# Optimization experiments

Measured on AMD Instinct MI355X. Metric: run time of the kernel, lower is better.

Reference implementation:

```python
import jax, jax.numpy as jnp
import numpy as np

N = 100000
E = 1600000
F_IN = 256
H1, C1 = 4, 32          # layer 1: heads=4, out_channels=32, concat=True -> 128
H2, C2 = 1, 16          # layer 2: heads=1, out_channels=nclass=16, concat=False
SLOPE = 0.2             # leaky relu negative slope


def setup_inputs() -> dict:
    key = jax.random.key(0)
    ks = jax.random.split(key, 10)
    x = jax.random.normal(ks[0], (N, F_IN), dtype=jnp.float32)
    row = jax.random.randint(ks[1], (E,), 0, N, dtype=jnp.int32)      # source j
    off = jax.random.randint(ks[2], (E,), 1, N, dtype=jnp.int32)
    col = ((row + off) % N).astype(jnp.int32)                          # target i, no self loops
    edge_index = jnp.stack([row, col])

    def glorot(k, shape, fan_in, fan_out):
        lim = np.sqrt(6.0 / (fan_in + fan_out))
        return jax.random.uniform(k, shape, jnp.float32, -lim, lim)

    W1 = glorot(ks[3], (F_IN, H1 * C1), F_IN, H1 * C1)
    att1 = glorot(ks[4], (1, H1, 2 * C1), H1, 2 * C1)
    b1 = jnp.zeros((H1 * C1,), jnp.float32)
    W2 = glorot(ks[5], (H1 * C1, H2 * C2), H1 * C1, H2 * C2)
    att2 = glorot(ks[6], (1, H2, 2 * C2), H2, 2 * C2)
    b2 = jnp.zeros((C2,), jnp.float32)
    return {"x": x, "edge_index": edge_index, "W1": W1, "att1": att1,
            "b1": b1, "W2": W2, "att2": att2, "b2": b2}


def gcn_norm(edge_index, num_nodes):
    # add_remaining_self_loops + symmetric normalization (GeoLayer.norm)
    loop = jnp.arange(num_nodes, dtype=edge_index.dtype)
    row = jnp.concatenate([edge_index[0], loop])
    col = jnp.concatenate([edge_index[1], loop])
    w = jnp.ones(row.shape[0], jnp.float32)
    deg = jax.ops.segment_sum(w, row, num_segments=num_nodes)
    dinv = jnp.where(deg > 0, jax.lax.rsqrt(deg), 0.0)
    return row, col, dinv[row] * w * dinv[col]


def segment_softmax(alpha, seg, num_segments):
    amax = jax.ops.segment_max(alpha, seg, num_segments=num_segments)
    ex = jnp.exp(alpha - amax[seg])
    denom = jax.ops.segment_sum(ex, seg, num_segments=num_segments)
    return ex / (denom[seg] + 1e-16)


def geo_layer(x, row, col, ew, W, att, b, heads, out_ch, concat):
    n = x.shape[0]
    xt = (x @ W).reshape(n, heads, out_ch)
    x_i = xt[col]                         # [E+N, H, C] target features
    x_j = xt[row]                         # [E+N, H, C] source features
    wl, wr = att[:, :, :out_ch], att[:, :, out_ch:]
    # (cat([x_i,x_j],-1) * att).sum(-1) == (x_i*wl).sum + (x_j*wr).sum
    alpha = (x_i * wl).sum(-1) + (x_j * wr).sum(-1)     # [E+N, H]
    alpha = jnp.where(alpha >= 0, alpha, SLOPE * alpha)  # leaky_relu
    alpha = segment_softmax(alpha, col, n)
    msg = ew[:, None, None] * x_j * alpha[:, :, None]    # [E+N, H, C]
    out = jax.ops.segment_sum(msg, col, num_segments=n)  # scatter-add to targets
    out = out.reshape(n, heads * out_ch) if concat else out.mean(axis=1)
    return out + b


def reference(x, edge_index, W1, att1, b1, W2, att2, b2):
    # norm is identical for both layers (edge_weight=None each time)
    row, col, ew = gcn_norm(edge_index, x.shape[0])
    h = geo_layer(x, row, col, ew, W1, att1, b1, H1, C1, True)
    h = jax.nn.relu(h)
    out = geo_layer(h, row, col, ew, W2, att2, b2, H2, C2, False)
    return out
```

## Files before the change

### kernel.cpp

```cpp
#include <hip/hip_runtime.h>
#include <math.h>

#define TPB 256
#define SEGN 512
#define SCAP 14336
#define CHB 8192
#define CAPC 12288

__device__ __forceinline__ float lrelu(float a){ return a >= 0.f ? a : 0.2f*a; }

typedef __attribute__((ext_vector_type(8))) short bf16x8;
typedef __attribute__((ext_vector_type(4))) float f32x4;

__device__ __forceinline__ unsigned short bfr(float f){
  unsigned u = __float_as_uint(f);
  return (unsigned short)((u + 0x7fffu + ((u >> 16) & 1u)) >> 16);
}

__device__ __forceinline__ void gl_lds16(const void* g, void* l){
  __builtin_amdgcn_global_load_lds(
      (const __attribute__((address_space(1))) void*)g,
      (__attribute__((address_space(3))) void*)l, 16, 0, 0);
}


__global__ __launch_bounds__(256) void k_bucket2(const int* __restrict__ rows, const int* __restrict__ cols,
    int* __restrict__ bcurC, int* __restrict__ bcurR,
    unsigned* __restrict__ ebufC, unsigned short* __restrict__ ebufR, int E, int NSEG2){
  __shared__ int lhist[256];
  __shared__ int lbase[256];
  int tid = threadIdx.x;
  int e0 = blockIdx.x * CHB;
  #pragma unroll 1
  for(int r=0; r<4; r++){
    lhist[tid] = 0;
    __syncthreads();
    int eb = e0 + r*2048;
    unsigned pk[8]; int sg[8], rk[8];
    #pragma unroll
    for(int i=0;i<8;i++){
      int e = eb + i*256 + tid;
      sg[i] = -1;
      if(e < E){
        int cc = cols[e], rr = rows[e];
        sg[i] = cc >> 9;
        pk[i] = ((unsigned)(cc & (SEGN-1)) << 17) | (unsigned)rr;
        rk[i] = atomicAdd(&lhist[sg[i]], 1);
      }
    }
    __syncthreads();
    if(tid < NSEG2){
      int c = lhist[tid];
      lbase[tid] = c ? atomicAdd(&bcurC[tid], c) : 0;
    }
    __syncthreads();
    #pragma unroll
    for(int i=0;i<8;i++)
      if(sg[i] >= 0){
        int p = lbase[sg[i]] + rk[i];
        if(p < CAPC) ebufC[sg[i]*CAPC + p] = pk[i];
      }
    __syncthreads();
  }
  #pragma unroll 1
  for(int r=0; r<4; r++){
    lhist[tid] = 0;
    __syncthreads();
    int eb = e0 + r*2048;
    int sg[8], rk[8]; unsigned short pv[8];
    #pragma unroll
    for(int i=0;i<8;i++){
      int e = eb + i*256 + tid;
      sg[i] = -1;
      if(e < E){
        int rr = rows[e];
        sg[i] = rr >> 9;
        pv[i] = (unsigned short)(rr & (SEGN-1));
        rk[i] = atomicAdd(&lhist[sg[i]], 1);
      }
    }
    __syncthreads();
    if(tid < NSEG2){
      int c = lhist[tid];
      lbase[tid] = c ? atomicAdd(&bcurR[tid], c) : 0;
    }
    __syncthreads();
    #pragma unroll
    for(int i=0;i<8;i++)
      if(sg[i] >= 0){
        int p = lbase[sg[i]] + rk[i];
        if(p < CAPC) ebufR[sg[i]*CAPC + p] = pv[i];
      }
    __syncthreads();
  }
}

__global__ __launch_bounds__(256) void k_cntseg(const int* __restrict__ bcurC, const int* __restrict__ bcurR,
    const unsigned* __restrict__ ebufC, const unsigned short* __restrict__ ebufR,
    int* __restrict__ cnt, float* __restrict__ dinv, int* __restrict__ bsum, int N){
  __shared__ int hc[SEGN];
  __shared__ int hr[SEGN];
  __shared__ int red[256];
  int s = blockIdx.x, tid = threadIdx.x;
  int lo = s*SEGN;
  int nn = min(SEGN, N - lo);
  for(int i=tid; i<SEGN; i+=256){ hc[i] = 0; hr[i] = 0; }
  __syncthreads();
  int cb = s*CAPC;
  int cc = min(bcurC[s], CAPC);
  int rc = min(bcurR[s], CAPC);
  for(int j=tid; j<cc; j+=256) atomicAdd(&hc[ebufC[cb + j] >> 17], 1);
  for(int j=tid; j<rc; j+=256) atomicAdd(&hr[ebufR[cb + j]], 1);
  __syncthreads();
  int tsum = 0;
  for(int i=tid; i<nn; i+=256){
    int c = hc[i] + 1;
    cnt[lo+i]  = c;
    tsum += c;
    dinv[lo+i] = 1.f / sqrtf((float)(hr[i] + 1));
  }
  red[tid] = tsum; __syncthreads();
  for(int off=128; off>0; off>>=1){
    if(tid < off) red[tid] += red[tid+off];
    __syncthreads();
  }
  if(tid == 0) bsum[s] = red[0];
}

__global__ void k_scan_bsum(int* bsum, int NB){
  __shared__ int s[256];
  int t = threadIdx.x;
  int v = (t < NB) ? bsum[t] : 0;
  s[t] = v; __syncthreads();
  for(int off=1; off<256; off<<=1){
    int add = (t >= off) ? s[t-off] : 0;
    __syncthreads();
    s[t] += add;
    __syncthreads();
  }
  if(t < NB) bsum[t] = s[t] - v;
}

__global__ void k_scan_write(const int* __restrict__ cnt, const int* __restrict__ bsum,
                             int* __restrict__ offs, int N){
  __shared__ int sdata[256];
  int t = threadIdx.x;
  int base = blockIdx.x*512 + t*2;
  int v0 = (base   < N) ? cnt[base]   : 0;
  int v1 = (base+1 < N) ? cnt[base+1] : 0;
  int s = v0 + v1;
  sdata[t] = s; __syncthreads();
  int mine = s;
  for(int off=1; off<256; off<<=1){
    int add = (t >= off) ? sdata[t-off] : 0;
    __syncthreads();
    sdata[t] += add;
    __syncthreads();
  }
  int run = sdata[t] - mine + bsum[blockIdx.x];
  if(base < N){
    offs[base] = run; run += v0;
    if(base == N-1) offs[N] = run;
  }
  if(base+1 < N){
    offs[base+1] = run; run += v1;
    if(base+1 == N-1) offs[N] = run;
  }
}

__global__ __launch_bounds__(256) void k_sortfill(const int* __restrict__ offs,
    const int* __restrict__ bcurC, const unsigned* __restrict__ ebuf,
    int* __restrict__ csr, int N){
  __shared__ int lcur[SEGN];
  __shared__ int lbuf[SCAP];
  int s = blockIdx.x, tid = threadIdx.x;
  int lo = s*SEGN;
  int nn = min(SEGN, N - lo);
  int base = offs[lo];
  int total = offs[lo+nn] - base;
  int eb = s*CAPC;
  int ec = min(bcurC[s], CAPC);
  if(total <= SCAP){
    for(int li=tid; li<nn; li+=256){
      int o = offs[lo+li] - base;
      lbuf[o]  = lo + li;
      lcur[li] = o + 1;
    }
    __syncthreads();
    for(int j=tid; j<ec; j+=256){
      unsigned pk = ebuf[eb + j];
      int li  = pk >> 17;
      int row = pk & 0x1FFFF;
      int p = atomicAdd(&lcur[li], 1);
      lbuf[p] = row;
    }
    __syncthreads();
    for(int j=tid; j<total; j+=256) csr[base + j] = lbuf[j];
  } else {
    for(int li=tid; li<nn; li+=256){
      int o = offs[lo+li];
      csr[o] = lo + li;
      lcur[li] = o + 1;
    }
    __syncthreads();
    for(int j=tid; j<ec; j+=256){
      unsigned pk = ebuf[eb + j];
      int li  = pk >> 17;
      int row = pk & 0x1FFFF;
      int p = atomicAdd(&lcur[li], 1);
      csr[p] = row;
    }
  }
}


__global__ void k_prepW(const float* __restrict__ W, short* __restrict__ Whi,
                        short* __restrict__ Wlo){
  int idx = blockIdx.x*256 + threadIdx.x;
  int n = idx >> 8, k = idx & 255;
  float f = W[k*128 + n];
  unsigned short h = bfr(f);
  float hf = __uint_as_float(((unsigned)h) << 16);
  Whi[n*256 + k] = (short)h;
  Wlo[n*256 + k] = (short)bfr(f - hf);
}


#define BUFB 24576
__global__ __launch_bounds__(256) void k_gemm1(
    const float* __restrict__ x,
    const short* __restrict__ Whi, const short* __restrict__ Wlo,
    const float* __restrict__ att1,
    unsigned* __restrict__ xtb, float* __restrict__ sl, float* __restrict__ sr, int N){
  __shared__ __align__(16) char smem[2*BUFB];
  float* fx = (float*)smem;
  float* att_sh = (float*)(smem + 17408);

  int tid = threadIdx.x;
  int n0 = blockIdx.x * 64;
  int w = tid >> 6, l = tid & 63;
  int wm = w & 1, wn = w >> 1;
  int lm = l & 15, lq = l >> 4;

  f32x4 acc[2][4];
  #pragma unroll
  for(int a=0;a<2;a++)
    #pragma unroll
    for(int b=0;b<4;b++) acc[a][b] = (f32x4){0.f,0.f,0.f,0.f};

  int ua0 = (w<<6) | l, ua1 = 256 + ua0;
  int ar0 = ua0 >> 3, as0 = (ua0 & 7) ^ (ar0 & 7);
  int ar1 = ua1 >> 3, as1 = (ua1 & 7) ^ (ar1 & 7);
  const float* gA0 = x + (size_t)min(n0 + ar0, N-1)*256 + as0*4;
  const float* gA1 = x + (size_t)min(n0 + ar1, N-1)*256 + as1*4;
  int ub0 = (w<<6) | l,  ub1 = 256 + ub0;
  int br0 = ub0 >> 2, bs0 = (ub0 & 3) ^ ((br0 >> 1) & 3);
  int br1 = ub1 >> 2, bs1 = (ub1 & 3) ^ ((br1 >> 1) & 3);
  const short* gBh0 = Whi + br0*256 + bs0*8;
  const short* gBh1 = Whi + br1*256 + bs1*8;
  const short* gBl0 = Wlo + br0*256 + bs0*8;
  const short* gBl1 = Wlo + br1*256 + bs1*8;
  int woff = w << 10;

  int offAf[2][2], offB[4];
  #pragma unroll
  for(int mt=0;mt<2;mt++){
    int rr = wm*32 + mt*16 + lm;
    offAf[mt][0] = rr*32 + (((2*lq+0) ^ (rr&7)) << 2);
    offAf[mt][1] = rr*32 + (((2*lq+1) ^ (rr&7)) << 2);
  }
  #pragma unroll
  for(int nt=0;nt<4;nt++){
    int rr = wn*64 + nt*16 + lm;
    offB[nt] = rr*32 + ((lq ^ ((rr>>1)&3)) << 3);
  }

  {
    char* base = smem;
    gl_lds16(gA0,  base          + woff);
    gl_lds16(gA1,  base + 4096   + woff);
    gl_lds16(gBh0, base + 8192   + woff);
    gl_lds16(gBh1, base + 12288  + woff);
    gl_lds16(gBl0, base + 16384  + woff);
    gl_lds16(gBl1, base + 20480  + woff);
  }
  __syncthreads();

  int cur = 0;
  #pragma unroll 1
  for(int c=0;c<8;c++){
    if(c < 7){
      int kf = (c+1) << 5;
      char* base = smem + (cur^1)*BUFB;
      gl_lds16(gA0  + kf, base          + woff);
      gl_lds16(gA1  + kf, base + 4096   + woff);
      gl_lds16(gBh0 + kf, base + 8192   + woff);
      gl_lds16(gBh1 + kf, base + 12288  + woff);
      gl_lds16(gBl0 + kf, base + 16384  + woff);
      gl_lds16(gBl1 + kf, base + 20480  + woff);
    }
    float* Axf = (float*)(smem + cur*BUFB);
    short* Bh  = (short*)(smem + cur*BUFB + 8192);
    short* Bl  = (short*)(smem + cur*BUFB + 16384);
    bf16x8 ah[2], al2[2];
    #pragma unroll
    for(int mt=0;mt<2;mt++){
      float4 f0 = *((const float4*)&Axf[offAf[mt][0]]);
      float4 f1 = *((const float4*)&Axf[offAf[mt][1]]);
      float fa[8] = {f0.x,f0.y,f0.z,f0.w,f1.x,f1.y,f1.z,f1.w};
      #pragma unroll
      for(int j=0;j<8;j++){
        unsigned short hb = bfr(fa[j]);
        float hf = __uint_as_float(((unsigned)hb) << 16);
        ah[mt][j]  = (short)hb;
        al2[mt][j] = (short)bfr(fa[j] - hf);
      }
    }
    #pragma unroll
    for(int nt=0;nt<4;nt++){
      bf16x8 bh = *((bf16x8*)&Bh[offB[nt]]);
      bf16x8 bl = *((bf16x8*)&Bl[offB[nt]]);
      #pragma unroll
      for(int mt=0;mt<2;mt++){
        acc[mt][nt] = __builtin_amdgcn_mfma_f32_16x16x32_bf16(ah[mt],  bh, acc[mt][nt], 0,0,0);
        acc[mt][nt] = __builtin_amdgcn_mfma_f32_16x16x32_bf16(ah[mt],  bl, acc[mt][nt], 0,0,0);
        acc[mt][nt] = __builtin_amdgcn_mfma_f32_16x16x32_bf16(al2[mt], bh, acc[mt][nt], 0,0,0);
      }
    }
    __syncthreads();
    cur ^= 1;
  }

  #pragma unroll
  for(int mt=0;mt<2;mt++){
    #pragma unroll
    for(int v=0;v<4;v++){
      int row = n0 + wm*32 + mt*16 + lq*4 + v;
      if(row < N){
        unsigned p0 = (unsigned)bfr(acc[mt][0][v]) | ((unsigned)bfr(acc[mt][2][v])<<16);
        unsigned p1 = (unsigned)bfr(acc[mt][1][v]) | ((unsigned)bfr(acc[mt][3][v])<<16);
        int jb = wn*32 + lm;
        xtb[(size_t)row*64 + jb]      = p0;
        xtb[(size_t)row*64 + jb + 16] = p1;
      }
    }
  }

  att_sh[tid] = att1[tid];
  #pragma unroll 1
  for(int p=0;p<2;p++){
    __syncthreads();
    if(wn == p){
      #pragma unroll
      for(int mt=0;mt<2;mt++)
        #pragma unroll
        for(int nt=0;nt<4;nt++)
          #pragma unroll
          for(int v=0;v<4;v++)
            fx[(wm*32 + mt*16 + lq*4 + v)*68 + nt*16 + lm] = acc[mt][nt][v];
    }
    __syncthreads();
    if(tid < 128){
      int rloc = tid >> 1, hh = tid & 1;
      int head = p*2 + hh;
      float a = 0.f, b = 0.f;
      #pragma unroll
      for(int c4=0;c4<8;c4++){
        float4 xv  = *((const float4*)&fx[rloc*68 + hh*32 + c4*4]);
        float4 alv = *((const float4*)&att_sh[head*64 + c4*4]);
        float4 arv = *((const float4*)&att_sh[head*64 + 32 + c4*4]);
        a += xv.x*alv.x + xv.y*alv.y + xv.z*alv.z + xv.w*alv.w;
        b += xv.x*arv.x + xv.y*arv.y + xv.z*arv.z + xv.w*arv.w;
      }
      int row = n0 + rloc;
      if(row < N){
        sl[(size_t)row*4 + head] = a;
        sr[(size_t)row*4 + head] = b;
      }
    }
  }
}


__global__ __launch_bounds__(64) void k_agg1(const int* __restrict__ offs, const int* __restrict__ srcs,
    const float* __restrict__ sl, const float* __restrict__ sr, const float* __restrict__ dinv,
    const unsigned* __restrict__ xtb, const float* __restrict__ b1, float* __restrict__ h, int N){
  __shared__ int   s_sh[64];
  __shared__ float w_sh[64*4];
  int n = blockIdx.x;
  if(n >= N) return;
  int lane = threadIdx.x;
  int beg = offs[n], end = offs[n+1];
  int deg = end - beg;
  float4 sln = *((const float4*)(sl + (size_t)n*4));
  int h0 = lane >> 5;
  float den0=0.f,den1=0.f,den2=0.f,den3=0.f;
  float acc0=0.f, acc1=0.f;

  if(deg <= 64){
    int j = beg + lane;
    int s = 0; float wd = 0.f;
    float a0=-1e30f, a1=-1e30f, a2=-1e30f, a3=-1e30f;
    if(j < end){
      s = srcs[j];
      float4 a = *((const float4*)(sr + (size_t)s*4));
      a0 = lrelu(sln.x + a.x);
      a1 = lrelu(sln.y + a.y);
      a2 = lrelu(sln.z + a.z);
      a3 = lrelu(sln.w + a.w);
      wd = dinv[s];
    }
    float m0=a0,m1=a1,m2=a2,m3=a3;
    #pragma unroll
    for(int o=32;o>0;o>>=1){
      m0 = fmaxf(m0, __shfl_xor(m0,o));
      m1 = fmaxf(m1, __shfl_xor(m1,o));
      m2 = fmaxf(m2, __shfl_xor(m2,o));
      m3 = fmaxf(m3, __shfl_xor(m3,o));
    }
    den0 = __expf(a0 - m0);
    den1 = __expf(a1 - m1);
    den2 = __expf(a2 - m2);
    den3 = __expf(a3 - m3);
    s_sh[lane] = s;
    w_sh[lane*4+0] = wd*den0;
    w_sh[lane*4+1] = wd*den1;
    w_sh[lane*4+2] = wd*den2;
    w_sh[lane*4+3] = wd*den3;
    __syncthreads();
    int k = 0;
    for(; k+8<=deg; k+=8){
      int sk[8];
      #pragma unroll
      for(int u=0;u<8;u++) sk[u] = __builtin_amdgcn_readfirstlane(s_sh[k+u]);
      unsigned pv[8];
      #pragma unroll
      for(int u=0;u<8;u++) pv[u] = xtb[(size_t)sk[u]*64 + lane];
      #pragma unroll
      for(int u=0;u<8;u++){
        float2 wv = *((const float2*)&w_sh[(k+u)*4 + h0*2]);
        acc0 += wv.x * __uint_as_float(pv[u] << 16);
        acc1 += wv.y * __uint_as_float(pv[u] & 0xffff0000u);
      }
    }
    for(; k<deg; k++){
      int sk = __builtin_amdgcn_readfirstlane(s_sh[k]);
      unsigned pvv = xtb[(size_t)sk*64 + lane];
      float2 wv = *((const float2*)&w_sh[k*4 + h0*2]);
      acc0 += wv.x * __uint_as_float(pvv << 16);
      acc1 += wv.y * __uint_as_float(pvv & 0xffff0000u);
    }
  } else {
    float m0=-1e30f,m1=-1e30f,m2=-1e30f,m3=-1e30f;
    for(int j=beg+lane; j<end; j+=64){
      int s = srcs[j];
      float4 a = *((const float4*)(sr + (size_t)s*4));
      m0 = fmaxf(m0, lrelu(sln.x + a.x));
      m1 = fmaxf(m1, lrelu(sln.y + a.y));
      m2 = fmaxf(m2, lrelu(sln.z + a.z));
      m3 = fmaxf(m3, lrelu(sln.w + a.w));
    }
    #pragma unroll
    for(int o=32;o>0;o>>=1){
      m0 = fmaxf(m0, __shfl_xor(m0,o));
      m1 = fmaxf(m1, __shfl_xor(m1,o));
      m2 = fmaxf(m2, __shfl_xor(m2,o));
      m3 = fmaxf(m3, __shfl_xor(m3,o));
    }
    for(int c0=beg; c0<end; c0+=64){
      int cnt = min(64, end-c0);
      int j = c0 + lane;
      float e0=0.f,e1=0.f,e2=0.f,e3=0.f, wd=0.f; int s=0;
      if(j<end){
        s = srcs[j];
        float4 a = *((const float4*)(sr + (size_t)s*4));
        e0 = __expf(lrelu(sln.x + a.x) - m0);
        e1 = __expf(lrelu(sln.y + a.y) - m1);
        e2 = __expf(lrelu(sln.z + a.z) - m2);
        e3 = __expf(lrelu(sln.w + a.w) - m3);
        wd = dinv[s];
      }
      den0+=e0; den1+=e1; den2+=e2; den3+=e3;
      s_sh[lane] = s;
      w_sh[lane*4+0] = wd*e0;
      w_sh[lane*4+1] = wd*e1;
      w_sh[lane*4+2] = wd*e2;
      w_sh[lane*4+3] = wd*e3;
      __syncthreads();
      int k = 0;
      for(; k+8<=cnt; k+=8){
        int sk[8];
        #pragma unroll
        for(int u=0;u<8;u++) sk[u] = __builtin_amdgcn_readfirstlane(s_sh[k+u]);
        unsigned pv[8];
        #pragma unroll
        for(int u=0;u<8;u++) pv[u] = xtb[(size_t)sk[u]*64 + lane];
        #pragma unroll
        for(int u=0;u<8;u++){
          float2 wv = *((const float2*)&w_sh[(k+u)*4 + h0*2]);
          acc0 += wv.x * __uint_as_float(pv[u] << 16);
          acc1 += wv.y * __uint_as_float(pv[u] & 0xffff0000u);
        }
      }
      for(; k<cnt; k++){
        int sk = __builtin_amdgcn_readfirstlane(s_sh[k]);
        unsigned pvv = xtb[(size_t)sk*64 + lane];
        float2 wv = *((const float2*)&w_sh[k*4 + h0*2]);
        acc0 += wv.x * __uint_as_float(pvv << 16);
        acc1 += wv.y * __uint_as_float(pvv & 0xffff0000u);
      }
      __syncthreads();
    }
  }
  #pragma unroll
  for(int o=32;o>0;o>>=1){
    den0 += __shfl_xor(den0,o);
    den1 += __shfl_xor(den1,o);
    den2 += __shfl_xor(den2,o);
    den3 += __shfl_xor(den3,o);
  }
  float din = dinv[n];
  int ch0 = (lane < 32) ? lane : lane + 32;
  int ch1 = ch0 + 32;
  float d0 = (lane < 32) ? den0 : den2;
  float d1 = (lane < 32) ? den1 : den3;
  float o0 = din*acc0/(d0 + 1e-16f) + b1[ch0];
  float o1 = din*acc1/(d1 + 1e-16f) + b1[ch1];
  h[(size_t)n*128 + ch0] = o0 > 0.f ? o0 : 0.f;
  h[(size_t)n*128 + ch1] = o1 > 0.f ? o1 : 0.f;
}


__global__ __launch_bounds__(256) void k_gemm2(const float* __restrict__ hmat, const float* __restrict__ W2,
    const float* __restrict__ att2, unsigned* __restrict__ xt2b,
    float* __restrict__ sl2, float* __restrict__ sr2, int N){
  __shared__ float hs[16*132];
  __shared__ float ws[16*132];
  __shared__ float xs[16*16];
  int t = threadIdx.x;
  int n0 = blockIdx.x * 16;
  #pragma unroll
  for(int i=0;i<8;i++){
    int idx = t + 256*i;
    int k = idx >> 4, c = idx & 15;
    ws[c*132 + k] = W2[idx];
  }
  #pragma unroll
  for(int i=0;i<2;i++){
    int idx = t + 256*i;
    int r = idx >> 5, k4 = idx & 31;
    int n = n0 + r;
    float4 v = make_float4(0.f,0.f,0.f,0.f);
    if(n < N) v = ((const float4*)hmat)[(size_t)n*32 + k4];
    *((float4*)&hs[r*132 + k4*4]) = v;
  }
  __syncthreads();
  int r = t >> 4, c = t & 15;
  float acc = 0.f;
  for(int k=0;k<128;k+=4){
    float4 hv = *((const float4*)&hs[r*132+k]);
    float4 wv = *((const float4*)&ws[c*132+k]);
    acc += hv.x*wv.x + hv.y*wv.y + hv.z*wv.z + hv.w*wv.w;
  }
  xs[r*16 + c] = acc;
  __syncthreads();
  int n = n0 + r;
  if(c < 8 && n < N){
    unsigned pk = (unsigned)bfr(xs[r*16+c]) | ((unsigned)bfr(xs[r*16+c+8])<<16);
    xt2b[(size_t)n*8 + c] = pk;
  }
  if(t < 16){
    int nn = n0 + t;
    if(nn < N){
      float a = 0.f, b = 0.f;
      #pragma unroll
      for(int cc=0;cc<16;cc++){ float v = xs[t*16+cc]; a += v*att2[cc]; b += v*att2[16+cc]; }
      sl2[nn] = a; sr2[nn] = b;
    }
  }
}


__global__ __launch_bounds__(64) void k_agg2(const int* __restrict__ offs, const int* __restrict__ srcs,
    const float* __restrict__ sl2, const float* __restrict__ sr2, const float* __restrict__ dinv,
    const unsigned* __restrict__ xt2b, const float* __restrict__ b2, float* __restrict__ out, int N){
  __shared__ int   s_sh[64];
  __shared__ float w_sh[64];
  int n = blockIdx.x;
  if(n >= N) return;
  int lane = threadIdx.x;
  int beg = offs[n], end = offs[n+1];
  int deg = end - beg;
  float sln = sl2[n];
  float den = 0.f, acc0 = 0.f, acc1 = 0.f;
  int grp = lane >> 3, ch = lane & 7;

  if(deg <= 64){
    int j = beg + lane;
    int s = 0; float wd = 0.f; float a = -1e30f;
    if(j < end){
      s = srcs[j];
      a = lrelu(sln + sr2[s]);
      wd = dinv[s];
    }
    float m = a;
    #pragma unroll
    for(int o=32;o>0;o>>=1) m = fmaxf(m, __shfl_xor(m,o));
    float e = __expf(a - m);
    den = e;
    s_sh[lane] = s;
    w_sh[lane] = wd*e;
    __syncthreads();
    for(int k=0;k<deg;k+=8){
      int kk = k + grp;
      if(kk < deg){
        int sk = s_sh[kk];
        float wk = w_sh[kk];
        unsigned pv = xt2b[(size_t)sk*8 + ch];
        acc0 += wk * __uint_as_float(pv << 16);
        acc1 += wk * __uint_as_float(pv & 0xffff0000u);
      }
    }
  } else {
    float m = -1e30f;
    for(int j=beg+lane; j<end; j+=64)
      m = fmaxf(m, lrelu(sln + sr2[srcs[j]]));
    #pragma unroll
    for(int o=32;o>0;o>>=1) m = fmaxf(m, __shfl_xor(m,o));
    for(int c0=beg; c0<end; c0+=64){
      int cnt = min(64, end-c0);
      int j = c0 + lane;
      float e=0.f, wd=0.f; int s=0;
      if(j<end){
        s = srcs[j];
        e = __expf(lrelu(sln + sr2[s]) - m);
        wd = dinv[s];
      }
      den += e;
      s_sh[lane] = s;
      w_sh[lane] = wd*e;
      __syncthreads();
      for(int k=0;k<cnt;k+=8){
        int kk = k + grp;
        if(kk < cnt){
          int sk = s_sh[kk];
          float wk = w_sh[kk];
          unsigned pv = xt2b[(size_t)sk*8 + ch];
          acc0 += wk * __uint_as_float(pv << 16);
          acc1 += wk * __uint_as_float(pv & 0xffff0000u);
        }
      }
      __syncthreads();
    }
  }
  #pragma unroll
  for(int o=32;o>0;o>>=1) den += __shfl_xor(den,o);
  acc0 += __shfl_xor(acc0,8);  acc0 += __shfl_xor(acc0,16);  acc0 += __shfl_xor(acc0,32);
  acc1 += __shfl_xor(acc1,8);  acc1 += __shfl_xor(acc1,16);  acc1 += __shfl_xor(acc1,32);
  if(lane < 8){
    float din = dinv[n];
    out[(size_t)n*16 + lane]     = din*acc0/(den + 1e-16f) + b2[lane];
    out[(size_t)n*16 + lane + 8] = din*acc1/(den + 1e-16f) + b2[lane+8];
  }
}


extern "C" void kernel_launch(void* const* d_in, const int* in_sizes, int n_in,
                              void* d_out, int out_size, void* d_ws, size_t ws_size,
                              hipStream_t stream){
  const float* x    = (const float*)d_in[0];
  const int*   ei   = (const int*)d_in[1];
  const float* W1   = (const float*)d_in[2];
  const float* att1 = (const float*)d_in[3];
  const float* b1   = (const float*)d_in[4];
  const float* W2   = (const float*)d_in[5];
  const float* att2 = (const float*)d_in[6];
  const float* b2   = (const float*)d_in[7];
  int N = in_sizes[0] / 256;
  int E = in_sizes[1] / 2;
  const int* rows = ei;
  const int* cols = ei + E;
  float* out = (float*)d_out;

  int ET    = E + N;
  int NSEG2 = (N + SEGN - 1) / SEGN;

  char* p = (char*)d_ws;
  auto alloc = [&](size_t bytes)->void*{ void* q = p; p += (bytes + 255) & ~(size_t)255; return q; };
  int*      cnt     = (int*)alloc((size_t)N*4);
  int*      offs    = (int*)alloc((size_t)(N+1)*4);
  int*      bsum    = (int*)alloc(256*4);
  int*      bcur    = (int*)alloc(512*4);
  int*      csr     = (int*)alloc((size_t)ET*4);
  float*    dinv    = (float*)alloc((size_t)N*4);
  unsigned* xtb     = (unsigned*)alloc((size_t)N*64*4);
  float*    sl1     = (float*)alloc((size_t)N*16);
  float*    sr1     = (float*)alloc((size_t)N*16);
  float*    hbuf    = (float*)alloc((size_t)N*128*4);
  unsigned* xt2b    = (unsigned*)alloc((size_t)N*8*4);
  float*    sl2     = (float*)alloc((size_t)N*4);
  float*    sr2     = (float*)alloc((size_t)N*4);
  short*    Whi     = (short*)alloc((size_t)128*256*2);
  short*    Wlo     = (short*)alloc((size_t)128*256*2);

  int* bcurC = bcur;
  int* bcurR = bcur + 256;

  unsigned*       ebufC = (unsigned*)xtb;
  unsigned short* ebufR = (unsigned short*)(ebufC + (size_t)NSEG2*CAPC);

  int gB = (E + CHB - 1) / CHB;

  hipMemsetAsync(bcur, 0, 512*4, stream);
  k_bucket2<<<gB, 256, 0, stream>>>(rows, cols, bcurC, bcurR, ebufC, ebufR, E, NSEG2);
  k_cntseg<<<NSEG2, 256, 0, stream>>>(bcurC, bcurR, ebufC, ebufR, cnt, dinv, bsum, N);
  k_scan_bsum<<<1, 256, 0, stream>>>(bsum, NSEG2);
  k_scan_write<<<NSEG2, 256, 0, stream>>>(cnt, bsum, offs, N);
  k_sortfill<<<NSEG2, 256, 0, stream>>>(offs, bcurC, ebufC, csr, N);

  k_prepW<<<128, 256, 0, stream>>>(W1, Whi, Wlo);
  k_gemm1<<<(N + 63)/64, 256, 0, stream>>>(x, Whi, Wlo, att1, xtb, sl1, sr1, N);
  k_agg1<<<N, 64, 0, stream>>>(offs, csr, sl1, sr1, dinv, xtb, b1, hbuf, N);

  k_gemm2<<<(N + 15)/16, 256, 0, stream>>>(hbuf, W2, att2, xt2b, sl2, sr2, N);
  k_agg2<<<N, 64, 0, stream>>>(offs, csr, sl2, sr2, dinv, xt2b, b2, out, N);
}
```

Measured before the change: 414.7 us.

## Fuse layer-2 GEMM into aggregation, merge bucketing passes and scan into sortfill

Three fusions. The layer-2 projection (h @ W2, the attention dot products and the bf16 packing) is computed per node inside k_agg1, so the 128-float hidden matrix is never written to or read back from global memory. The two bucketing passes over the edge list become a single pass that reads rows and cols once. The per-segment offset scan moves into the sortfill kernel, which removes a launch and a reread of offs. The cost is that each 64-thread agg1 block now reads all of W2 from global or cache, does an extra shuffle reduction and two more barriers, and uses more registers, which may reduce occupancy.

Measured after the change: 406.4 us. 1.02x faster.

```diff
diff --git a/kernel.cpp b/kernel.cpp
--- a/kernel.cpp
+++ b/kernel.cpp
@@ -24,72 +24,45 @@
 }
 
 
-__global__ __launch_bounds__(256) void k_bucket2(const int* __restrict__ rows, const int* __restrict__ cols,
+__global__ __launch_bounds__(256) void k_bucketM(const int* __restrict__ rows, const int* __restrict__ cols,
     int* __restrict__ bcurC, int* __restrict__ bcurR,
     unsigned* __restrict__ ebufC, unsigned short* __restrict__ ebufR, int E, int NSEG2){
-  __shared__ int lhist[256];
-  __shared__ int lbase[256];
+  __shared__ int lhC[256], lbC[256], lhR[256], lbR[256];
   int tid = threadIdx.x;
   int e0 = blockIdx.x * CHB;
   #pragma unroll 1
   for(int r=0; r<4; r++){
-    lhist[tid] = 0;
+    lhC[tid] = 0; lhR[tid] = 0;
     __syncthreads();
     int eb = e0 + r*2048;
-    unsigned pk[8]; int sg[8], rk[8];
+    unsigned pk[8]; int sgC[8], rkC[8], sgR[8], rkR[8]; int pvR[8];
     #pragma unroll
     for(int i=0;i<8;i++){
       int e = eb + i*256 + tid;
-      sg[i] = -1;
+      sgC[i] = -1;
       if(e < E){
         int cc = cols[e], rr = rows[e];
-        sg[i] = cc >> 9;
-        pk[i] = ((unsigned)(cc & (SEGN-1)) << 17) | (unsigned)rr;
-        rk[i] = atomicAdd(&lhist[sg[i]], 1);
+        sgC[i] = cc >> 9;
+        pk[i]  = ((unsigned)(cc & (SEGN-1)) << 17) | (unsigned)rr;
+        rkC[i] = atomicAdd(&lhC[sgC[i]], 1);
+        sgR[i] = rr >> 9;
+        pvR[i] = rr & (SEGN-1);
+        rkR[i] = atomicAdd(&lhR[sgR[i]], 1);
       }
     }
     __syncthreads();
     if(tid < NSEG2){
-      int c = lhist[tid];
-      lbase[tid] = c ? atomicAdd(&bcurC[tid], c) : 0;
+      int c = lhC[tid];  lbC[tid] = c  ? atomicAdd(&bcurC[tid], c)  : 0;
+      int c2 = lhR[tid]; lbR[tid] = c2 ? atomicAdd(&bcurR[tid], c2) : 0;
     }
     __syncthreads();
     #pragma unroll
     for(int i=0;i<8;i++)
-      if(sg[i] >= 0){
-        int p = lbase[sg[i]] + rk[i];
-        if(p < CAPC) ebufC[sg[i]*CAPC + p] = pk[i];
-      }
-    __syncthreads();
-  }
-  #pragma unroll 1
-  for(int r=0; r<4; r++){
-    lhist[tid] = 0;
-    __syncthreads();
-    int eb = e0 + r*2048;
-    int sg[8], rk[8]; unsigned short pv[8];
-    #pragma unroll
-    for(int i=0;i<8;i++){
-      int e = eb + i*256 + tid;
-      sg[i] = -1;
-      if(e < E){
-        int rr = rows[e];
-        sg[i] = rr >> 9;
-        pv[i] = (unsigned short)(rr & (SEGN-1));
-        rk[i] = atomicAdd(&lhist[sg[i]], 1);
-      }
-    }
-    __syncthreads();
-    if(tid < NSEG2){
-      int c = lhist[tid];
-      lbase[tid] = c ? atomicAdd(&bcurR[tid], c) : 0;
-    }
-    __syncthreads();
-    #pragma unroll
-    for(int i=0;i<8;i++)
-      if(sg[i] >= 0){
-        int p = lbase[sg[i]] + rk[i];
-        if(p < CAPC) ebufR[sg[i]*CAPC + p] = pv[i];
+      if(sgC[i] >= 0){
+        int p = lbC[sgC[i]] + rkC[i];
+        if(p < CAPC) ebufC[sgC[i]*CAPC + p] = pk[i];
+        int p2 = lbR[sgR[i]] + rkR[i];
+        if(p2 < CAPC) ebufR[sgR[i]*CAPC + p2] = (unsigned short)pvR[i];
       }
     __syncthreads();
   }
@@ -141,50 +114,46 @@
   if(t < NB) bsum[t] = s[t] - v;
 }
 
-__global__ void k_scan_write(const int* __restrict__ cnt, const int* __restrict__ bsum,
-                             int* __restrict__ offs, int N){
-  __shared__ int sdata[256];
-  int t = threadIdx.x;
-  int base = blockIdx.x*512 + t*2;
-  int v0 = (base   < N) ? cnt[base]   : 0;
-  int v1 = (base+1 < N) ? cnt[base+1] : 0;
-  int s = v0 + v1;
-  sdata[t] = s; __syncthreads();
-  int mine = s;
-  for(int off=1; off<256; off<<=1){
-    int add = (t >= off) ? sdata[t-off] : 0;
-    __syncthreads();
-    sdata[t] += add;
-    __syncthreads();
-  }
-  int run = sdata[t] - mine + bsum[blockIdx.x];
-  if(base < N){
-    offs[base] = run; run += v0;
-    if(base == N-1) offs[N] = run;
-  }
-  if(base+1 < N){
-    offs[base+1] = run; run += v1;
-    if(base+1 == N-1) offs[N] = run;
-  }
-}
-
-__global__ __launch_bounds__(256) void k_sortfill(const int* __restrict__ offs,
-    const int* __restrict__ bcurC, const unsigned* __restrict__ ebuf,
+__global__ __launch_bounds__(256) void k_sortfill2(const int* __restrict__ cnt,
+    const int* __restrict__ bsum, const int* __restrict__ bcurC,
+    const unsigned* __restrict__ ebuf, int* __restrict__ offs,
     int* __restrict__ csr, int N){
   __shared__ int lcur[SEGN];
   __shared__ int lbuf[SCAP];
+  __shared__ int sdata[256];
   int s = blockIdx.x, tid = threadIdx.x;
   int lo = s*SEGN;
   int nn = min(SEGN, N - lo);
-  int base = offs[lo];
-  int total = offs[lo+nn] - base;
+  int base = bsum[s];
+  int i0 = tid*2, i1 = i0+1;
+  int v0 = (i0 < nn) ? cnt[lo+i0] : 0;
+  int v1 = (i1 < nn) ? cnt[lo+i1] : 0;
+  int ssum = v0 + v1;
+  sdata[tid] = ssum; __syncthreads();
+  int mine = ssum;
+  for(int off=1; off<256; off<<=1){
+    int add = (tid >= off) ? sdata[tid-off] : 0;
+    __syncthreads();
+    sdata[tid] += add;
+    __syncthreads();
+  }
+  int total = sdata[255];
+  int run0 = sdata[tid] - mine;
+  int run1 = run0 + v0;
   int eb = s*CAPC;
   int ec = min(bcurC[s], CAPC);
   if(total <= SCAP){
-    for(int li=tid; li<nn; li+=256){
-      int o = offs[lo+li] - base;
-      lbuf[o]  = lo + li;
-      lcur[li] = o + 1;
+    if(i0 < nn){
+      offs[lo+i0] = base + run0;
+      lbuf[run0]  = lo + i0;
+      lcur[i0]    = run0 + 1;
+      if(lo+i0 == N-1) offs[N] = base + run0 + v0;
+    }
+    if(i1 < nn){
+      offs[lo+i1] = base + run1;
+      lbuf[run1]  = lo + i1;
+      lcur[i1]    = run1 + 1;
+      if(lo+i1 == N-1) offs[N] = base + run1 + v1;
     }
     __syncthreads();
     for(int j=tid; j<ec; j+=256){
@@ -197,10 +166,17 @@
     __syncthreads();
     for(int j=tid; j<total; j+=256) csr[base + j] = lbuf[j];
   } else {
-    for(int li=tid; li<nn; li+=256){
-      int o = offs[lo+li];
-      csr[o] = lo + li;
-      lcur[li] = o + 1;
+    if(i0 < nn){
+      offs[lo+i0] = base + run0;
+      csr[base+run0] = lo + i0;
+      lcur[i0] = base + run0 + 1;
+      if(lo+i0 == N-1) offs[N] = base + run0 + v0;
+    }
+    if(i1 < nn){
+      offs[lo+i1] = base + run1;
+      csr[base+run1] = lo + i1;
+      lcur[i1] = base + run1 + 1;
+      if(lo+i1 == N-1) offs[N] = base + run1 + v1;
     }
     __syncthreads();
     for(int j=tid; j<ec; j+=256){
@@ -384,9 +360,12 @@
 
 __global__ __launch_bounds__(64) void k_agg1(const int* __restrict__ offs, const int* __restrict__ srcs,
     const float* __restrict__ sl, const float* __restrict__ sr, const float* __restrict__ dinv,
-    const unsigned* __restrict__ xtb, const float* __restrict__ b1, float* __restrict__ h, int N){
+    const unsigned* __restrict__ xtb, const float* __restrict__ b1,
+    const float* __restrict__ W2, const float* __restrict__ att2,
+    float* __restrict__ sl2, float* __restrict__ sr2, unsigned* __restrict__ xt2b, int N){
   __shared__ int   s_sh[64];
   __shared__ float w_sh[64*4];
+  __shared__ float h_sh[144];
   int n = blockIdx.x;
   if(n >= N) return;
   int lane = threadIdx.x;
@@ -526,57 +505,46 @@
   float d1 = (lane < 32) ? den1 : den3;
   float o0 = din*acc0/(d0 + 1e-16f) + b1[ch0];
   float o1 = din*acc1/(d1 + 1e-16f) + b1[ch1];
-  h[(size_t)n*128 + ch0] = o0 > 0.f ? o0 : 0.f;
-  h[(size_t)n*128 + ch1] = o1 > 0.f ? o1 : 0.f;
-}
-
-
-__global__ __launch_bounds__(256) void k_gemm2(const float* __restrict__ hmat, const float* __restrict__ W2,
-    const float* __restrict__ att2, unsigned* __restrict__ xt2b,
-    float* __restrict__ sl2, float* __restrict__ sr2, int N){
-  __shared__ float hs[16*132];
-  __shared__ float ws[16*132];
-  __shared__ float xs[16*16];
-  int t = threadIdx.x;
-  int n0 = blockIdx.x * 16;
-  #pragma unroll
-  for(int i=0;i<8;i++){
-    int idx = t + 256*i;
-    int k = idx >> 4, c = idx & 15;
-    ws[c*132 + k] = W2[idx];
-  }
-  #pragma unroll
-  for(int i=0;i<2;i++){
-    int idx = t + 256*i;
-    int r = idx >> 5, k4 = idx & 31;
-    int n = n0 + r;
-    float4 v = make_float4(0.f,0.f,0.f,0.f);
-    if(n < N) v = ((const float4*)hmat)[(size_t)n*32 + k4];
-    *((float4*)&hs[r*132 + k4*4]) = v;
-  }
+  o0 = o0 > 0.f ? o0 : 0.f;
+  o1 = o1 > 0.f ? o1 : 0.f;
+
+  h_sh[ch0] = o0;
+  h_sh[ch1] = o1;
   __syncthreads();
-  int r = t >> 4, c = t & 15;
-  float acc = 0.f;
-  for(int k=0;k<128;k+=4){
-    float4 hv = *((const float4*)&hs[r*132+k]);
-    float4 wv = *((const float4*)&ws[c*132+k]);
-    acc += hv.x*wv.x + hv.y*wv.y + hv.z*wv.z + hv.w*wv.w;
-  }
-  xs[r*16 + c] = acc;
+  int c4 = lane & 3, q = lane >> 2;
+  const float4* W24 = (const float4*)W2;
+  f32x4 a4 = (f32x4){0.f,0.f,0.f,0.f};
+  #pragma unroll
+  for(int j=0;j<8;j++){
+    int k = q*8 + j;
+    float hv = h_sh[k];
+    float4 wv = W24[k*4 + c4];
+    a4[0] += hv*wv.x; a4[1] += hv*wv.y; a4[2] += hv*wv.z; a4[3] += hv*wv.w;
+  }
+  #pragma unroll
+  for(int o=4;o<64;o<<=1){
+    a4[0] += __shfl_xor(a4[0],o);
+    a4[1] += __shfl_xor(a4[1],o);
+    a4[2] += __shfl_xor(a4[2],o);
+    a4[3] += __shfl_xor(a4[3],o);
+  }
+  if(lane < 4){
+    h_sh[128 + lane*4 + 0] = a4[0];
+    h_sh[128 + lane*4 + 1] = a4[1];
+    h_sh[128 + lane*4 + 2] = a4[2];
+    h_sh[128 + lane*4 + 3] = a4[3];
+  }
   __syncthreads();
-  int n = n0 + r;
-  if(c < 8 && n < N){
-    unsigned pk = (unsigned)bfr(xs[r*16+c]) | ((unsigned)bfr(xs[r*16+c+8])<<16);
-    xt2b[(size_t)n*8 + c] = pk;
-  }
-  if(t < 16){
-    int nn = n0 + t;
-    if(nn < N){
-      float a = 0.f, b = 0.f;
-      #pragma unroll
-      for(int cc=0;cc<16;cc++){ float v = xs[t*16+cc]; a += v*att2[cc]; b += v*att2[16+cc]; }
-      sl2[nn] = a; sr2[nn] = b;
-    }
+  if(lane < 16){
+    float v = h_sh[128 + lane];
+    float t0 = v*att2[lane], t1 = v*att2[16 + lane];
+    #pragma unroll
+    for(int o=1;o<16;o<<=1){ t0 += __shfl_xor(t0,o); t1 += __shfl_xor(t1,o); }
+    if(lane == 0){ sl2[n] = t0; sr2[n] = t1; }
+  }
+  if(lane < 8){
+    unsigned pk = (unsigned)bfr(h_sh[128+lane]) | ((unsigned)bfr(h_sh[128+lane+8])<<16);
+    xt2b[(size_t)n*8 + lane] = pk;
   }
 }
 
@@ -696,7 +664,6 @@
   unsigned* xtb     = (unsigned*)alloc((size_t)N*64*4);
   float*    sl1     = (float*)alloc((size_t)N*16);
   float*    sr1     = (float*)alloc((size_t)N*16);
-  float*    hbuf    = (float*)alloc((size_t)N*128*4);
   unsigned* xt2b    = (unsigned*)alloc((size_t)N*8*4);
   float*    sl2     = (float*)alloc((size_t)N*4);
   float*    sr2     = (float*)alloc((size_t)N*4);
@@ -712,16 +679,13 @@
   int gB = (E + CHB - 1) / CHB;
 
   hipMemsetAsync(bcur, 0, 512*4, stream);
-  k_bucket2<<<gB, 256, 0, stream>>>(rows, cols, bcurC, bcurR, ebufC, ebufR, E, NSEG2);
+  k_bucketM<<<gB, 256, 0, stream>>>(rows, cols, bcurC, bcurR, ebufC, ebufR, E, NSEG2);
   k_cntseg<<<NSEG2, 256, 0, stream>>>(bcurC, bcurR, ebufC, ebufR, cnt, dinv, bsum, N);
   k_scan_bsum<<<1, 256, 0, stream>>>(bsum, NSEG2);
-  k_scan_write<<<NSEG2, 256, 0, stream>>>(cnt, bsum, offs, N);
-  k_sortfill<<<NSEG2, 256, 0, stream>>>(offs, bcurC, ebufC, csr, N);
+  k_sortfill2<<<NSEG2, 256, 0, stream>>>(cnt, bsum, bcurC, ebufC, offs, csr, N);
 
   k_prepW<<<128, 256, 0, stream>>>(W1, Whi, Wlo);
   k_gemm1<<<(N + 63)/64, 256, 0, stream>>>(x, Whi, Wlo, att1, xtb, sl1, sr1, N);
-  k_agg1<<<N, 64, 0, stream>>>(offs, csr, sl1, sr1, dinv, xtb, b1, hbuf, N);
-
-  k_gemm2<<<(N + 15)/16, 256, 0, stream>>>(hbuf, W2, att2, xt2b, sl2, sr2, N);
+  k_agg1<<<N, 64, 0, stream>>>(offs, csr, sl1, sr1, dinv, xtb, b1, W2, att2, sl2, sr2, xt2b, N);
   k_agg2<<<N, 64, 0, stream>>>(offs, csr, sl2, sr2, dinv, xt2b, b2, out, N);
 }
```
